# Kernel tuning notes

Measured on AMD Instinct MI355X. Metric: run time of the kernel, lower is better.

## Reference

```python
import jax, jax.numpy as jnp
import numpy as np

WS = 7          # window size (Wh == Ww)
NUM_HEADS = 4

def _relative_position_index(ws):
    coords = np.stack(np.meshgrid(np.arange(ws), np.arange(ws), indexing='ij'))  # (2, ws, ws)
    cf = coords.reshape(2, -1)                                # (2, N)
    rel = cf[:, :, None] - cf[:, None, :]                     # (2, N, N)
    rel = rel.transpose(1, 2, 0)                              # (N, N, 2)
    rel[:, :, 0] += ws - 1
    rel[:, :, 1] += ws - 1
    rel[:, :, 0] *= 2 * ws - 1
    return rel.sum(-1)                                        # (N, N) int

REL_IDX = jnp.asarray(_relative_position_index(WS))


def setup_inputs() -> dict:
    key = jax.random.key(0)
    ks = jax.random.split(key, 7)
    B, C, H, W = 4096, 128, WS, WS
    nW = 64
    N = H * W
    return {
        'x': jax.random.normal(ks[0], (B, C, H, W), jnp.float32),
        'mask': jax.random.normal(ks[1], (nW, 1, N, N), jnp.float32),
        'qkv_w': jax.random.normal(ks[2], (3 * C, C), jnp.float32) * 0.02,
        'qkv_b': jax.random.normal(ks[3], (3 * C,), jnp.float32) * 0.02,
        'proj_w': jax.random.normal(ks[4], (C, C), jnp.float32) * 0.02,
        'proj_b': jax.random.normal(ks[5], (C,), jnp.float32) * 0.02,
        'bias_table': jax.random.normal(ks[6], ((2 * WS - 1) ** 2, NUM_HEADS), jnp.float32) * 0.02,
    }


def reference(x, mask, qkv_w, qkv_b, proj_w, proj_b, bias_table):
    B, C, H, W = x.shape
    N = H * W
    heads = NUM_HEADS
    hd = C // heads
    scale = jnp.asarray(hd, x.dtype) ** -0.5

    # 1x1 conv qkv: (B,C,H,W) -> (B,3C,H,W), then to (B,N,3C)
    qkv = jnp.einsum('bchw,oc->bhwo', x, qkv_w) + qkv_b      # (B,H,W,3C)
    qkv = qkv.reshape(B, N, 3, heads, hd)                     # split channel into q/k/v
    q, k, v = (qkv[:, :, i].transpose(0, 2, 1, 3) for i in range(3))  # each (B,heads,N,hd)

    attn = jnp.einsum('bhnd,bhmd->bhnm', q * scale, k)        # (B,heads,N,N)

    rel_bias = bias_table[REL_IDX.reshape(-1)].reshape(N, N, heads)
    attn = attn + rel_bias.transpose(2, 0, 1)[None]           # (1,heads,N,N) broadcast

    nW = mask.shape[0]
    attn = attn + jnp.tile(mask, (B // nW, 1, 1, 1))          # (B,1,N,N) broadcast over heads

    attn = jax.nn.softmax(attn, axis=-1)
    out = jnp.einsum('bhnm,bhmd->bhnd', attn, v)              # (B,heads,N,hd)
    out = out.transpose(0, 2, 1, 3).reshape(B, N, C)          # (B,N,C)
    out = out.transpose(0, 2, 1).reshape(B, C, H, W)

    # 1x1 proj conv
    out = jnp.einsum('bchw,oc->bohw', out, proj_w) + proj_b[None, :, None, None]
    return out
```

## Files before the change

### kernel.cpp

```cpp
#include <hip/hip_runtime.h>

typedef __attribute__((ext_vector_type(8))) short short8;
typedef __attribute__((ext_vector_type(4))) float f32x4;
typedef __attribute__((ext_vector_type(4))) unsigned short bfu4;

#define MFMA(a, b, c) __builtin_amdgcn_mfma_f32_16x16x32_bf16((a), (b), (c), 0, 0, 0)

__device__ __forceinline__ unsigned short f2bf(float f) {
    union { float f; unsigned u; } v; v.f = f;
    unsigned r = v.u + 0x7fffu + ((v.u >> 16) & 1u);
    return (unsigned short)(r >> 16);
}

__global__ __launch_bounds__(256)
void prep_kernel(const float* __restrict__ qkv_w, const float* __restrict__ proj_w,
                 unsigned short* __restrict__ wf)
{
    int id = blockIdx.x * 256 + threadIdx.x;
    int j  = id & 7;
    int l  = (id >> 3) & 63;
    int ks = (id >> 9) & 3;
    int row16 = l & 15;
    int kk = ks * 32 + ((l >> 4) << 3) + j;
    if (id < 49152) {
        int mt = id >> 11;
        wf[id] = f2bf(qkv_w[(mt * 16 + row16) * 128 + kk]);
    } else {
        int mt = (id - 49152) >> 11;
        wf[id] = f2bf(proj_w[(mt * 16 + row16) * 128 + kk]);
    }
}

#define XS 0
#define QKO 16384
#define VTO 49152
#define PPO 0
#define AOO 32768
#define LDS_BYTES 65536
#define SCALE 0.17677669529663687f

__global__ __launch_bounds__(256, 2)
void win_attn_mfma(const float* __restrict__ x, const float* __restrict__ mask,
                   const float* __restrict__ qkv_b, const float* __restrict__ proj_b,
                   const float* __restrict__ bt, const unsigned short* __restrict__ wf,
                   float* __restrict__ out)
{
    extern __shared__ char smem[];
    const int b = blockIdx.x, tid = threadIdx.x;
    const int w = tid >> 6, l = tid & 63, g = l >> 4, lr = l & 15;

    const float* xb = x + (size_t)b * 6272;
    for (int r = tid; r < 6272; r += 256) {
        int c = (int)(((unsigned)r * 21400u) >> 20);
        int n = r - c * 49;
        int byte = n * 256 + ((c * 2) ^ ((n & 7) << 4));
        *(unsigned short*)(smem + XS + byte) = f2bf(xb[r]);
    }
    for (int i = tid; i < 1920; i += 256) {
        int n = 49 + (i >> 7), c = i & 127;
        int byte = n * 256 + ((c * 2) ^ ((n & 7) << 4));
        *(unsigned short*)(smem + XS + byte) = 0;
    }
    __syncthreads();

    const short8* wfa = (const short8*)wf;

    {
        f32x4 acc[6][4];
        #pragma unroll
        for (int mt = 0; mt < 6; ++mt)
            #pragma unroll
            for (int nt = 0; nt < 4; ++nt) acc[mt][nt] = (f32x4){0.f, 0.f, 0.f, 0.f};

        #pragma unroll
        for (int ks = 0; ks < 4; ++ks) {
            short8 aF[6], bF[4];
            #pragma unroll
            for (int mt = 0; mt < 6; ++mt)
                aF[mt] = wfa[((w * 6 + mt) * 4 + ks) * 64 + l];
            #pragma unroll
            for (int nt = 0; nt < 4; ++nt) {
                int n = nt * 16 + lr;
                int byte = n * 256 + (((ks * 32 + g * 8) * 2) ^ ((n & 7) << 4));
                bF[nt] = *(const short8*)(smem + XS + byte);
            }
            #pragma unroll
            for (int mt = 0; mt < 6; ++mt)
                #pragma unroll
                for (int nt = 0; nt < 4; ++nt)
                    acc[mt][nt] = MFMA(aF[mt], bF[nt], acc[mt][nt]);
        }

        #pragma unroll
        for (int mt = 0; mt < 6; ++mt) {
            int o0 = w * 96 + mt * 16;
            f32x4 bias = *(const f32x4*)(qkv_b + o0 + g * 4);
            #pragma unroll
            for (int nt = 0; nt < 4; ++nt) acc[mt][nt] += bias;

            if (o0 < 128) {
                int hh = o0 >> 5, dl = (o0 & 31) + g * 4;
                #pragma unroll
                for (int nt = 0; nt < 4; ++nt) {
                    int n = nt * 16 + lr;
                    bfu4 u;
                    #pragma unroll
                    for (int r2 = 0; r2 < 4; ++r2) u[r2] = f2bf(acc[mt][nt][r2] * SCALE);
                    int byte = hh * 8192 + n * 128 + ((dl * 2) ^ ((n & 7) << 4));
                    *(bfu4*)(smem + QKO + byte) = u;
                }
            } else if (o0 < 256) {
                int o2 = o0 - 128, hh = o2 >> 5, dl = (o2 & 31) + g * 4;
                #pragma unroll
                for (int nt = 0; nt < 4; ++nt) {
                    int n = nt * 16 + lr;
                    bfu4 u;
                    #pragma unroll
                    for (int r2 = 0; r2 < 4; ++r2) u[r2] = f2bf(acc[mt][nt][r2]);
                    int byte = hh * 8192 + n * 128 + ((64 + dl * 2) ^ ((n & 7) << 4));
                    *(bfu4*)(smem + QKO + byte) = u;
                }
            } else {
                int o2 = o0 - 256, hh = o2 >> 5, dl = (o2 & 31) + g * 4;
                #pragma unroll
                for (int nt = 0; nt < 4; ++nt) {
                    int m = nt * 16 + lr;
                    #pragma unroll
                    for (int r2 = 0; r2 < 4; ++r2) {
                        int d = dl + r2;
                        int byte = hh * 4096 + d * 128 + ((m * 2) ^ ((d & 7) << 4));
                        *(unsigned short*)(smem + VTO + byte) = f2bf(acc[mt][nt][r2]);
                    }
                }
            }
        }
    }
    __syncthreads();

    const int h = w, wi = b & 63;
    f32x4 S[4][4];

    {
        int pm[4], mc[4]; bool mv[4];
        #pragma unroll
        for (int nt = 0; nt < 4; ++nt) {
            int m = nt * 16 + lr;
            int m_c = m > 48 ? 48 : m;
            int ym = (m_c * 147) >> 10, xm = m_c - ym * 7;
            pm[nt] = ym * 13 + xm; mc[nt] = m_c; mv[nt] = (m < 49);
        }
        const float* mrow = mask + (size_t)wi * 2401;
        #pragma unroll
        for (int mt = 0; mt < 4; ++mt) {
            #pragma unroll
            for (int r2 = 0; r2 < 4; ++r2) {
                int n = mt * 16 + g * 4 + r2;
                int n_c = n > 48 ? 48 : n;
                int yn = (n_c * 147) >> 10, xn = n_c - yn * 7;
                int pn = yn * 13 + xn;
                const float* mr2 = mrow + n_c * 49;
                #pragma unroll
                for (int nt = 0; nt < 4; ++nt) {
                    S[mt][nt][r2] = mv[nt]
                        ? (mr2[mc[nt]] + bt[(pn - pm[nt] + 84) * 4 + h])
                        : -1e30f;
                }
            }
        }
    }

    {
        short8 qF[4], kF[4];
        #pragma unroll
        for (int t = 0; t < 4; ++t) {
            int n = t * 16 + lr;
            int rb2 = h * 8192 + n * 128, sw = (n & 7) << 4;
            qF[t] = *(const short8*)(smem + QKO + rb2 + ((g * 16) ^ sw));
            kF[t] = *(const short8*)(smem + QKO + rb2 + ((64 + g * 16) ^ sw));
        }
        #pragma unroll
        for (int mt = 0; mt < 4; ++mt)
            #pragma unroll
            for (int nt = 0; nt < 4; ++nt)
                S[mt][nt] = MFMA(qF[mt], kF[nt], S[mt][nt]);
    }

    #pragma unroll
    for (int mt = 0; mt < 4; ++mt) {
        f32x4 mx = S[mt][0];
        #pragma unroll
        for (int nt = 1; nt < 4; ++nt)
            #pragma unroll
            for (int r2 = 0; r2 < 4; ++r2) mx[r2] = fmaxf(mx[r2], S[mt][nt][r2]);
        #pragma unroll
        for (int r2 = 0; r2 < 4; ++r2) {
            float v2 = mx[r2];
            v2 = fmaxf(v2, __shfl_xor(v2, 1));
            v2 = fmaxf(v2, __shfl_xor(v2, 2));
            v2 = fmaxf(v2, __shfl_xor(v2, 4));
            v2 = fmaxf(v2, __shfl_xor(v2, 8));
            mx[r2] = v2;
        }
        f32x4 sum = (f32x4){0.f, 0.f, 0.f, 0.f};
        #pragma unroll
        for (int nt = 0; nt < 4; ++nt)
            #pragma unroll
            for (int r2 = 0; r2 < 4; ++r2) {
                float e = __expf(S[mt][nt][r2] - mx[r2]);
                S[mt][nt][r2] = e; sum[r2] += e;
            }
        #pragma unroll
        for (int r2 = 0; r2 < 4; ++r2) {
            float s2 = sum[r2];
            s2 += __shfl_xor(s2, 1);
            s2 += __shfl_xor(s2, 2);
            s2 += __shfl_xor(s2, 4);
            s2 += __shfl_xor(s2, 8);
            sum[r2] = 1.0f / s2;
        }
        #pragma unroll
        for (int nt = 0; nt < 4; ++nt)
            #pragma unroll
            for (int r2 = 0; r2 < 4; ++r2) S[mt][nt][r2] *= sum[r2];
    }
    __syncthreads();

    #pragma unroll
    for (int mt = 0; mt < 4; ++mt)
        #pragma unroll
        for (int r2 = 0; r2 < 4; ++r2) {
            int n = mt * 16 + g * 4 + r2;
            int rowb = h * 8192 + n * 128, sw = (n & 7) << 4;
            #pragma unroll
            for (int nt = 0; nt < 4; ++nt) {
                int m = nt * 16 + lr;
                *(unsigned short*)(smem + PPO + rowb + ((m * 2) ^ sw)) = f2bf(S[mt][nt][r2]);
            }
        }

    f32x4 O[4][2];
    #pragma unroll
    for (int mt = 0; mt < 4; ++mt)
        #pragma unroll
        for (int nt2 = 0; nt2 < 2; ++nt2) O[mt][nt2] = (f32x4){0.f, 0.f, 0.f, 0.f};
    #pragma unroll
    for (int ks2 = 0; ks2 < 2; ++ks2) {
        short8 pF[4], vF[2];
        #pragma unroll
        for (int mt = 0; mt < 4; ++mt) {
            int n = mt * 16 + lr;
            pF[mt] = *(const short8*)(smem + PPO + h * 8192 + n * 128 +
                                      ((ks2 * 64 + g * 16) ^ ((n & 7) << 4)));
        }
        #pragma unroll
        for (int nt2 = 0; nt2 < 2; ++nt2) {
            int d = nt2 * 16 + lr;
            vF[nt2] = *(const short8*)(smem + VTO + h * 4096 + d * 128 +
                                       ((ks2 * 64 + g * 16) ^ ((d & 7) << 4)));
        }
        #pragma unroll
        for (int mt = 0; mt < 4; ++mt)
            #pragma unroll
            for (int nt2 = 0; nt2 < 2; ++nt2)
                O[mt][nt2] = MFMA(pF[mt], vF[nt2], O[mt][nt2]);
    }
    #pragma unroll
    for (int mt = 0; mt < 4; ++mt)
        #pragma unroll
        for (int nt2 = 0; nt2 < 2; ++nt2)
            #pragma unroll
            for (int r2 = 0; r2 < 4; ++r2) {
                int n = mt * 16 + g * 4 + r2;
                int c = h * 32 + nt2 * 16 + lr;
                *(unsigned short*)(smem + AOO + n * 256 + ((c * 2) ^ ((n & 7) << 4))) =
                    f2bf(O[mt][nt2][r2]);
            }
    __syncthreads();

    f32x4 Pa[4][2];
    #pragma unroll
    for (int mt = 0; mt < 4; ++mt)
        #pragma unroll
        for (int ct = 0; ct < 2; ++ct) Pa[mt][ct] = (f32x4){0.f, 0.f, 0.f, 0.f};
    #pragma unroll
    for (int ks = 0; ks < 4; ++ks) {
        short8 aF[4], bF[2];
        #pragma unroll
        for (int mt = 0; mt < 4; ++mt) {
            int n = mt * 16 + lr;
            aF[mt] = *(const short8*)(smem + AOO + n * 256 +
                                      (((ks * 32 + g * 8) * 2) ^ ((n & 7) << 4)));
        }
        #pragma unroll
        for (int ct = 0; ct < 2; ++ct)
            bF[ct] = wfa[6144 + ((w * 2 + ct) * 4 + ks) * 64 + l];
        #pragma unroll
        for (int mt = 0; mt < 4; ++mt)
            #pragma unroll
            for (int ct = 0; ct < 2; ++ct)
                Pa[mt][ct] = MFMA(aF[mt], bF[ct], Pa[mt][ct]);
    }
    float* ob = out + (size_t)b * 6272;
    #pragma unroll
    for (int ct = 0; ct < 2; ++ct) {
        int co = (w * 2 + ct) * 16 + lr;
        float pb2 = proj_b[co];
        #pragma unroll
        for (int mt = 0; mt < 4; ++mt) {
            int n0 = mt * 16 + g * 4;
            if (mt < 3) {
                #pragma unroll
                for (int r2 = 0; r2 < 4; ++r2)
                    ob[co * 49 + n0 + r2] = Pa[mt][ct][r2] + pb2;
            } else if (g == 0) {
                ob[co * 49 + 48] = Pa[3][ct][0] + pb2;
            }
        }
    }
}

extern "C" void kernel_launch(void* const* d_in, const int* in_sizes, int n_in,
                              void* d_out, int out_size, void* d_ws, size_t ws_size,
                              hipStream_t stream) {
    const float* x      = (const float*)d_in[0];
    const float* mask   = (const float*)d_in[1];
    const float* qkv_w  = (const float*)d_in[2];
    const float* qkv_b  = (const float*)d_in[3];
    const float* proj_w = (const float*)d_in[4];
    const float* proj_b = (const float*)d_in[5];
    const float* btab   = (const float*)d_in[6];
    float* o = (float*)d_out;
    unsigned short* wf = (unsigned short*)d_ws;

    prep_kernel<<<256, 256, 0, stream>>>(qkv_w, proj_w, wf);

    hipFuncSetAttribute(reinterpret_cast<const void*>(win_attn_mfma),
                        hipFuncAttributeMaxDynamicSharedMemorySize, LDS_BYTES);
    win_attn_mfma<<<4096, 256, LDS_BYTES, stream>>>(x, mask, qkv_b, proj_b, btab, wf, o);
}
```

Measured before the change: 173.6 us.

## Process heads in two passes to shrink LDS and double occupancy

Restructures the window attention kernel to compute QKV and attention for two heads per pass, with each wave handling half the query rows of one head. The LDS footprint drops from 64KB to 40KB and launch bounds rise to 4 blocks per CU, targeting higher occupancy and latency hiding. The x load is also vectorised to float4, and the attention output is kept in registers across passes before the projection. The cost is more barriers per block and a second QKV GEMM pass that reloads x fragments, with a risk of register pressure under the tighter launch bound.

```diff
diff --git a/kernel.cpp b/kernel.cpp
--- a/kernel.cpp
+++ b/kernel.cpp
@@ -5,6 +5,7 @@
 typedef __attribute__((ext_vector_type(4))) unsigned short bfu4;
 
 #define MFMA(a, b, c) __builtin_amdgcn_mfma_f32_16x16x32_bf16((a), (b), (c), 0, 0, 0)
+#define SCALE 0.17677669529663687f
 
 __device__ __forceinline__ unsigned short f2bf(float f) {
     union { float f; unsigned u; } v; v.f = f;
@@ -13,8 +14,8 @@
 }
 
 __global__ __launch_bounds__(256)
-void prep_kernel(const float* __restrict__ qkv_w, const float* __restrict__ proj_w,
-                 unsigned short* __restrict__ wf)
+void prep_w(const float* __restrict__ qkv_w, const float* __restrict__ proj_w,
+            unsigned short* __restrict__ wf)
 {
     int id = blockIdx.x * 256 + threadIdx.x;
     int j  = id & 7;
@@ -31,15 +32,11 @@
     }
 }
 
-#define XS 0
 #define QKO 16384
-#define VTO 49152
-#define PPO 0
-#define AOO 32768
-#define LDS_BYTES 65536
-#define SCALE 0.17677669529663687f
-
-__global__ __launch_bounds__(256, 2)
+#define VTO2 32768
+#define LDS_BYTES 40960
+
+__global__ __launch_bounds__(256, 4)
 void win_attn_mfma(const float* __restrict__ x, const float* __restrict__ mask,
                    const float* __restrict__ qkv_b, const float* __restrict__ proj_b,
                    const float* __restrict__ bt, const unsigned short* __restrict__ wf,
@@ -48,248 +45,269 @@
     extern __shared__ char smem[];
     const int b = blockIdx.x, tid = threadIdx.x;
     const int w = tid >> 6, l = tid & 63, g = l >> 4, lr = l & 15;
-
-    const float* xb = x + (size_t)b * 6272;
-    for (int r = tid; r < 6272; r += 256) {
-        int c = (int)(((unsigned)r * 21400u) >> 20);
-        int n = r - c * 49;
-        int byte = n * 256 + ((c * 2) ^ ((n & 7) << 4));
-        *(unsigned short*)(smem + XS + byte) = f2bf(xb[r]);
-    }
-    for (int i = tid; i < 1920; i += 256) {
-        int n = 49 + (i >> 7), c = i & 127;
-        int byte = n * 256 + ((c * 2) ^ ((n & 7) << 4));
-        *(unsigned short*)(smem + XS + byte) = 0;
+    const int wi = b & 63;
+    const int hh = w >> 1;
+    const int nh = w & 1;
+
+    {
+        const float4* xb4 = (const float4*)(x + (size_t)b * 6272);
+        for (int i = tid; i < 1568; i += 256) {
+            float4 v4 = xb4[i];
+            float vals[4] = {v4.x, v4.y, v4.z, v4.w};
+            int r0 = i * 4;
+            #pragma unroll
+            for (int e = 0; e < 4; ++e) {
+                int r = r0 + e;
+                int c = (int)(((unsigned)r * 21400u) >> 20);
+                int n = r - c * 49;
+                *(unsigned short*)(smem + n * 256 + ((c * 2) ^ ((n & 7) << 4))) =
+                    f2bf(vals[e]);
+            }
+        }
+        for (int i = tid; i < 1920; i += 256) {
+            int n = 49 + (i >> 7), c = i & 127;
+            *(unsigned short*)(smem + n * 256 + ((c * 2) ^ ((n & 7) << 4))) = 0;
+        }
     }
     __syncthreads();
 
     const short8* wfa = (const short8*)wf;
-
-    {
-        f32x4 acc[6][4];
-        #pragma unroll
-        for (int mt = 0; mt < 6; ++mt)
-            #pragma unroll
-            for (int nt = 0; nt < 4; ++nt) acc[mt][nt] = (f32x4){0.f, 0.f, 0.f, 0.f};
-
-        #pragma unroll
-        for (int ks = 0; ks < 4; ++ks) {
-            short8 aF[6], bF[4];
-            #pragma unroll
-            for (int mt = 0; mt < 6; ++mt)
-                aF[mt] = wfa[((w * 6 + mt) * 4 + ks) * 64 + l];
-            #pragma unroll
-            for (int nt = 0; nt < 4; ++nt) {
-                int n = nt * 16 + lr;
-                int byte = n * 256 + (((ks * 32 + g * 8) * 2) ^ ((n & 7) << 4));
-                bF[nt] = *(const short8*)(smem + XS + byte);
-            }
-            #pragma unroll
-            for (int mt = 0; mt < 6; ++mt)
-                #pragma unroll
-                for (int nt = 0; nt < 4; ++nt)
-                    acc[mt][nt] = MFMA(aF[mt], bF[nt], acc[mt][nt]);
-        }
-
-        #pragma unroll
-        for (int mt = 0; mt < 6; ++mt) {
-            int o0 = w * 96 + mt * 16;
-            f32x4 bias = *(const f32x4*)(qkv_b + o0 + g * 4);
-            #pragma unroll
-            for (int nt = 0; nt < 4; ++nt) acc[mt][nt] += bias;
-
-            if (o0 < 128) {
-                int hh = o0 >> 5, dl = (o0 & 31) + g * 4;
+    f32x4 Osav[2][2][2];
+
+    #pragma unroll
+    for (int p2 = 0; p2 < 2; ++p2) {
+        #pragma unroll
+        for (int i = 0; i < 3; ++i) {
+            const int j = w * 3 + i;
+            const int typ = j >> 2;
+            const int jj = j & 3;
+            const int ph = jj >> 1;
+            const int blk = jj & 1;
+            const int T = typ * 8 + p2 * 4 + jj;
+            const int ob = T * 16;
+
+            short8 af[4];
+            #pragma unroll
+            for (int ks = 0; ks < 4; ++ks) af[ks] = wfa[(T * 4 + ks) * 64 + l];
+            f32x4 acc[4];
+            #pragma unroll
+            for (int nt = 0; nt < 4; ++nt) acc[nt] = (f32x4){0.f, 0.f, 0.f, 0.f};
+            #pragma unroll
+            for (int ks = 0; ks < 4; ++ks) {
+                #pragma unroll
+                for (int nt = 0; nt < 4; ++nt) {
+                    int n = nt * 16 + lr;
+                    short8 xf = *(const short8*)(smem + n * 256 +
+                                    ((ks * 64 + g * 16) ^ ((n & 7) << 4)));
+                    acc[nt] = MFMA(af[ks], xf, acc[nt]);
+                }
+            }
+            f32x4 bv = *(const f32x4*)(qkv_b + ob + g * 4);
+            #pragma unroll
+            for (int nt = 0; nt < 4; ++nt) acc[nt] += bv;
+
+            if (typ == 0) {
                 #pragma unroll
                 for (int nt = 0; nt < 4; ++nt) {
                     int n = nt * 16 + lr;
                     bfu4 u;
                     #pragma unroll
-                    for (int r2 = 0; r2 < 4; ++r2) u[r2] = f2bf(acc[mt][nt][r2] * SCALE);
-                    int byte = hh * 8192 + n * 128 + ((dl * 2) ^ ((n & 7) << 4));
-                    *(bfu4*)(smem + QKO + byte) = u;
-                }
-            } else if (o0 < 256) {
-                int o2 = o0 - 128, hh = o2 >> 5, dl = (o2 & 31) + g * 4;
+                    for (int r2 = 0; r2 < 4; ++r2) u[r2] = f2bf(acc[nt][r2] * SCALE);
+                    *(bfu4*)(smem + QKO + ph * 8192 + n * 128 +
+                             ((blk * 32 + g * 8) ^ ((n & 7) << 4))) = u;
+                }
+            } else if (typ == 1) {
                 #pragma unroll
                 for (int nt = 0; nt < 4; ++nt) {
                     int n = nt * 16 + lr;
                     bfu4 u;
                     #pragma unroll
-                    for (int r2 = 0; r2 < 4; ++r2) u[r2] = f2bf(acc[mt][nt][r2]);
-                    int byte = hh * 8192 + n * 128 + ((64 + dl * 2) ^ ((n & 7) << 4));
-                    *(bfu4*)(smem + QKO + byte) = u;
+                    for (int r2 = 0; r2 < 4; ++r2) u[r2] = f2bf(acc[nt][r2]);
+                    *(bfu4*)(smem + QKO + ph * 8192 + n * 128 +
+                             ((64 + blk * 32 + g * 8) ^ ((n & 7) << 4))) = u;
                 }
             } else {
-                int o2 = o0 - 256, hh = o2 >> 5, dl = (o2 & 31) + g * 4;
                 #pragma unroll
                 for (int nt = 0; nt < 4; ++nt) {
                     int m = nt * 16 + lr;
                     #pragma unroll
                     for (int r2 = 0; r2 < 4; ++r2) {
-                        int d = dl + r2;
-                        int byte = hh * 4096 + d * 128 + ((m * 2) ^ ((d & 7) << 4));
-                        *(unsigned short*)(smem + VTO + byte) = f2bf(acc[mt][nt][r2]);
+                        int d = blk * 16 + g * 4 + r2;
+                        *(unsigned short*)(smem + VTO2 + ph * 4096 + d * 128 +
+                                           ((m * 2) ^ ((d & 7) << 4))) = f2bf(acc[nt][r2]);
                     }
                 }
             }
         }
-    }
-    __syncthreads();
-
-    const int h = w, wi = b & 63;
-    f32x4 S[4][4];
-
-    {
-        int pm[4], mc[4]; bool mv[4];
-        #pragma unroll
-        for (int nt = 0; nt < 4; ++nt) {
-            int m = nt * 16 + lr;
-            int m_c = m > 48 ? 48 : m;
-            int ym = (m_c * 147) >> 10, xm = m_c - ym * 7;
-            pm[nt] = ym * 13 + xm; mc[nt] = m_c; mv[nt] = (m < 49);
-        }
-        const float* mrow = mask + (size_t)wi * 2401;
-        #pragma unroll
-        for (int mt = 0; mt < 4; ++mt) {
-            #pragma unroll
-            for (int r2 = 0; r2 < 4; ++r2) {
-                int n = mt * 16 + g * 4 + r2;
-                int n_c = n > 48 ? 48 : n;
-                int yn = (n_c * 147) >> 10, xn = n_c - yn * 7;
-                int pn = yn * 13 + xn;
-                const float* mr2 = mrow + n_c * 49;
-                #pragma unroll
-                for (int nt = 0; nt < 4; ++nt) {
-                    S[mt][nt][r2] = mv[nt]
-                        ? (mr2[mc[nt]] + bt[(pn - pm[nt] + 84) * 4 + h])
-                        : -1e30f;
-                }
-            }
-        }
-    }
-
-    {
-        short8 qF[4], kF[4];
-        #pragma unroll
-        for (int t = 0; t < 4; ++t) {
-            int n = t * 16 + lr;
-            int rb2 = h * 8192 + n * 128, sw = (n & 7) << 4;
-            qF[t] = *(const short8*)(smem + QKO + rb2 + ((g * 16) ^ sw));
-            kF[t] = *(const short8*)(smem + QKO + rb2 + ((64 + g * 16) ^ sw));
-        }
-        #pragma unroll
-        for (int mt = 0; mt < 4; ++mt)
-            #pragma unroll
-            for (int nt = 0; nt < 4; ++nt)
-                S[mt][nt] = MFMA(qF[mt], kF[nt], S[mt][nt]);
-    }
-
-    #pragma unroll
-    for (int mt = 0; mt < 4; ++mt) {
-        f32x4 mx = S[mt][0];
-        #pragma unroll
-        for (int nt = 1; nt < 4; ++nt)
-            #pragma unroll
-            for (int r2 = 0; r2 < 4; ++r2) mx[r2] = fmaxf(mx[r2], S[mt][nt][r2]);
-        #pragma unroll
-        for (int r2 = 0; r2 < 4; ++r2) {
-            float v2 = mx[r2];
-            v2 = fmaxf(v2, __shfl_xor(v2, 1));
-            v2 = fmaxf(v2, __shfl_xor(v2, 2));
-            v2 = fmaxf(v2, __shfl_xor(v2, 4));
-            v2 = fmaxf(v2, __shfl_xor(v2, 8));
-            mx[r2] = v2;
-        }
-        f32x4 sum = (f32x4){0.f, 0.f, 0.f, 0.f};
-        #pragma unroll
-        for (int nt = 0; nt < 4; ++nt)
-            #pragma unroll
-            for (int r2 = 0; r2 < 4; ++r2) {
-                float e = __expf(S[mt][nt][r2] - mx[r2]);
-                S[mt][nt][r2] = e; sum[r2] += e;
-            }
-        #pragma unroll
-        for (int r2 = 0; r2 < 4; ++r2) {
-            float s2 = sum[r2];
-            s2 += __shfl_xor(s2, 1);
-            s2 += __shfl_xor(s2, 2);
-            s2 += __shfl_xor(s2, 4);
-            s2 += __shfl_xor(s2, 8);
-            sum[r2] = 1.0f / s2;
-        }
-        #pragma unroll
-        for (int nt = 0; nt < 4; ++nt)
-            #pragma unroll
-            for (int r2 = 0; r2 < 4; ++r2) S[mt][nt][r2] *= sum[r2];
-    }
-    __syncthreads();
-
-    #pragma unroll
-    for (int mt = 0; mt < 4; ++mt)
-        #pragma unroll
-        for (int r2 = 0; r2 < 4; ++r2) {
-            int n = mt * 16 + g * 4 + r2;
-            int rowb = h * 8192 + n * 128, sw = (n & 7) << 4;
+        __syncthreads();
+
+        const int hgl = p2 * 2 + hh;
+        f32x4 S[2][4];
+        {
+            int pm[4], mc[4]; bool mv[4];
             #pragma unroll
             for (int nt = 0; nt < 4; ++nt) {
                 int m = nt * 16 + lr;
-                *(unsigned short*)(smem + PPO + rowb + ((m * 2) ^ sw)) = f2bf(S[mt][nt][r2]);
-            }
-        }
-
-    f32x4 O[4][2];
+                int m_c = m > 48 ? 48 : m;
+                int ym = (m_c * 147) >> 10, xm = m_c - ym * 7;
+                pm[nt] = ym * 13 + xm; mc[nt] = m_c; mv[nt] = (m < 49);
+            }
+            const float* mrow = mask + (size_t)wi * 2401;
+            #pragma unroll
+            for (int mt = 0; mt < 2; ++mt) {
+                #pragma unroll
+                for (int r2 = 0; r2 < 4; ++r2) {
+                    int n = nh * 32 + mt * 16 + g * 4 + r2;
+                    int n_c = n > 48 ? 48 : n;
+                    int yn = (n_c * 147) >> 10, xn = n_c - yn * 7;
+                    int pn = yn * 13 + xn;
+                    const float* mr2 = mrow + n_c * 49;
+                    #pragma unroll
+                    for (int nt = 0; nt < 4; ++nt) {
+                        S[mt][nt][r2] = mv[nt]
+                            ? (mr2[mc[nt]] + bt[(pn - pm[nt] + 84) * 4 + hgl])
+                            : -1e30f;
+                    }
+                }
+            }
+        }
+        {
+            short8 qF[2], kF[4];
+            #pragma unroll
+            for (int t = 0; t < 2; ++t) {
+                int n = nh * 32 + t * 16 + lr;
+                qF[t] = *(const short8*)(smem + QKO + hh * 8192 + n * 128 +
+                                         ((g * 16) ^ ((n & 7) << 4)));
+            }
+            #pragma unroll
+            for (int t = 0; t < 4; ++t) {
+                int m = t * 16 + lr;
+                kF[t] = *(const short8*)(smem + QKO + hh * 8192 + m * 128 +
+                                         ((64 + g * 16) ^ ((m & 7) << 4)));
+            }
+            #pragma unroll
+            for (int mt = 0; mt < 2; ++mt)
+                #pragma unroll
+                for (int nt = 0; nt < 4; ++nt)
+                    S[mt][nt] = MFMA(qF[mt], kF[nt], S[mt][nt]);
+        }
+        #pragma unroll
+        for (int mt = 0; mt < 2; ++mt) {
+            f32x4 mx = S[mt][0];
+            #pragma unroll
+            for (int nt = 1; nt < 4; ++nt)
+                #pragma unroll
+                for (int r2 = 0; r2 < 4; ++r2) mx[r2] = fmaxf(mx[r2], S[mt][nt][r2]);
+            #pragma unroll
+            for (int r2 = 0; r2 < 4; ++r2) {
+                float v2 = mx[r2];
+                v2 = fmaxf(v2, __shfl_xor(v2, 1));
+                v2 = fmaxf(v2, __shfl_xor(v2, 2));
+                v2 = fmaxf(v2, __shfl_xor(v2, 4));
+                v2 = fmaxf(v2, __shfl_xor(v2, 8));
+                mx[r2] = v2;
+            }
+            f32x4 sum = (f32x4){0.f, 0.f, 0.f, 0.f};
+            #pragma unroll
+            for (int nt = 0; nt < 4; ++nt)
+                #pragma unroll
+                for (int r2 = 0; r2 < 4; ++r2) {
+                    float e = __expf(S[mt][nt][r2] - mx[r2]);
+                    S[mt][nt][r2] = e; sum[r2] += e;
+                }
+            #pragma unroll
+            for (int r2 = 0; r2 < 4; ++r2) {
+                float s2 = sum[r2];
+                s2 += __shfl_xor(s2, 1);
+                s2 += __shfl_xor(s2, 2);
+                s2 += __shfl_xor(s2, 4);
+                s2 += __shfl_xor(s2, 8);
+                sum[r2] = 1.0f / s2;
+            }
+            #pragma unroll
+            for (int nt = 0; nt < 4; ++nt)
+                #pragma unroll
+                for (int r2 = 0; r2 < 4; ++r2) S[mt][nt][r2] *= sum[r2];
+        }
+        __syncthreads();
+
+        #pragma unroll
+        for (int mt = 0; mt < 2; ++mt)
+            #pragma unroll
+            for (int r2 = 0; r2 < 4; ++r2) {
+                int n = nh * 32 + mt * 16 + g * 4 + r2;
+                int rowb = QKO + hh * 8192 + n * 128, sw = (n & 7) << 4;
+                #pragma unroll
+                for (int nt = 0; nt < 4; ++nt) {
+                    int m = nt * 16 + lr;
+                    *(unsigned short*)(smem + rowb + ((m * 2) ^ sw)) =
+                        f2bf(S[mt][nt][r2]);
+                }
+            }
+        __syncthreads();
+
+        f32x4 O[2][2];
+        #pragma unroll
+        for (int mt = 0; mt < 2; ++mt)
+            #pragma unroll
+            for (int dt = 0; dt < 2; ++dt) O[mt][dt] = (f32x4){0.f, 0.f, 0.f, 0.f};
+        #pragma unroll
+        for (int ks2 = 0; ks2 < 2; ++ks2) {
+            short8 pf[2], vf[2];
+            #pragma unroll
+            for (int mt = 0; mt < 2; ++mt) {
+                int n = nh * 32 + mt * 16 + lr;
+                pf[mt] = *(const short8*)(smem + QKO + hh * 8192 + n * 128 +
+                                          ((ks2 * 64 + g * 16) ^ ((n & 7) << 4)));
+            }
+            #pragma unroll
+            for (int dt = 0; dt < 2; ++dt) {
+                int d = dt * 16 + lr;
+                vf[dt] = *(const short8*)(smem + VTO2 + hh * 4096 + d * 128 +
+                                          ((ks2 * 64 + g * 16) ^ ((d & 7) << 4)));
+            }
+            #pragma unroll
+            for (int mt = 0; mt < 2; ++mt)
+                #pragma unroll
+                for (int dt = 0; dt < 2; ++dt)
+                    O[mt][dt] = MFMA(pf[mt], vf[dt], O[mt][dt]);
+        }
+        #pragma unroll
+        for (int mt = 0; mt < 2; ++mt)
+            #pragma unroll
+            for (int dt = 0; dt < 2; ++dt) Osav[p2][mt][dt] = O[mt][dt];
+        __syncthreads();
+    }
+
+    #pragma unroll
+    for (int p2 = 0; p2 < 2; ++p2)
+        #pragma unroll
+        for (int mt = 0; mt < 2; ++mt)
+            #pragma unroll
+            for (int dt = 0; dt < 2; ++dt) {
+                int c = (p2 * 2 + hh) * 32 + dt * 16 + lr;
+                #pragma unroll
+                for (int r2 = 0; r2 < 4; ++r2) {
+                    int n = nh * 32 + mt * 16 + g * 4 + r2;
+                    *(unsigned short*)(smem + n * 256 + ((c * 2) ^ ((n & 7) << 4))) =
+                        f2bf(Osav[p2][mt][dt][r2]);
+                }
+            }
+    __syncthreads();
+
+    f32x4 Pa[4][2];
     #pragma unroll
     for (int mt = 0; mt < 4; ++mt)
         #pragma unroll
-        for (int nt2 = 0; nt2 < 2; ++nt2) O[mt][nt2] = (f32x4){0.f, 0.f, 0.f, 0.f};
-    #pragma unroll
-    for (int ks2 = 0; ks2 < 2; ++ks2) {
-        short8 pF[4], vF[2];
+        for (int ct = 0; ct < 2; ++ct) Pa[mt][ct] = (f32x4){0.f, 0.f, 0.f, 0.f};
+    #pragma unroll
+    for (int ks = 0; ks < 4; ++ks) {
+        short8 aF[4], bF[2];
         #pragma unroll
         for (int mt = 0; mt < 4; ++mt) {
             int n = mt * 16 + lr;
-            pF[mt] = *(const short8*)(smem + PPO + h * 8192 + n * 128 +
-                                      ((ks2 * 64 + g * 16) ^ ((n & 7) << 4)));
-        }
-        #pragma unroll
-        for (int nt2 = 0; nt2 < 2; ++nt2) {
-            int d = nt2 * 16 + lr;
-            vF[nt2] = *(const short8*)(smem + VTO + h * 4096 + d * 128 +
-                                       ((ks2 * 64 + g * 16) ^ ((d & 7) << 4)));
-        }
-        #pragma unroll
-        for (int mt = 0; mt < 4; ++mt)
-            #pragma unroll
-            for (int nt2 = 0; nt2 < 2; ++nt2)
-                O[mt][nt2] = MFMA(pF[mt], vF[nt2], O[mt][nt2]);
-    }
-    #pragma unroll
-    for (int mt = 0; mt < 4; ++mt)
-        #pragma unroll
-        for (int nt2 = 0; nt2 < 2; ++nt2)
-            #pragma unroll
-            for (int r2 = 0; r2 < 4; ++r2) {
-                int n = mt * 16 + g * 4 + r2;
-                int c = h * 32 + nt2 * 16 + lr;
-                *(unsigned short*)(smem + AOO + n * 256 + ((c * 2) ^ ((n & 7) << 4))) =
-                    f2bf(O[mt][nt2][r2]);
-            }
-    __syncthreads();
-
-    f32x4 Pa[4][2];
-    #pragma unroll
-    for (int mt = 0; mt < 4; ++mt)
-        #pragma unroll
-        for (int ct = 0; ct < 2; ++ct) Pa[mt][ct] = (f32x4){0.f, 0.f, 0.f, 0.f};
-    #pragma unroll
-    for (int ks = 0; ks < 4; ++ks) {
-        short8 aF[4], bF[2];
-        #pragma unroll
-        for (int mt = 0; mt < 4; ++mt) {
-            int n = mt * 16 + lr;
-            aF[mt] = *(const short8*)(smem + AOO + n * 256 +
-                                      (((ks * 32 + g * 8) * 2) ^ ((n & 7) << 4)));
+            aF[mt] = *(const short8*)(smem + n * 256 +
+                          ((ks * 64 + g * 16) ^ ((n & 7) << 4)));
         }
         #pragma unroll
         for (int ct = 0; ct < 2; ++ct)
@@ -300,7 +318,7 @@
             for (int ct = 0; ct < 2; ++ct)
                 Pa[mt][ct] = MFMA(aF[mt], bF[ct], Pa[mt][ct]);
     }
-    float* ob = out + (size_t)b * 6272;
+    float* obp = out + (size_t)b * 6272;
     #pragma unroll
     for (int ct = 0; ct < 2; ++ct) {
         int co = (w * 2 + ct) * 16 + lr;
@@ -311,9 +329,9 @@
             if (mt < 3) {
                 #pragma unroll
                 for (int r2 = 0; r2 < 4; ++r2)
-                    ob[co * 49 + n0 + r2] = Pa[mt][ct][r2] + pb2;
+                    obp[co * 49 + n0 + r2] = Pa[mt][ct][r2] + pb2;
             } else if (g == 0) {
-                ob[co * 49 + 48] = Pa[3][ct][0] + pb2;
+                obp[co * 49 + 48] = Pa[3][ct][0] + pb2;
             }
         }
     }
@@ -330,11 +348,12 @@
     const float* proj_b = (const float*)d_in[5];
     const float* btab   = (const float*)d_in[6];
     float* o = (float*)d_out;
+
     unsigned short* wf = (unsigned short*)d_ws;
 
-    prep_kernel<<<256, 256, 0, stream>>>(qkv_w, proj_w, wf);
-
-    hipFuncSetAttribute(reinterpret_cast<const void*>(win_attn_mfma),
+    prep_w<<<256, 256, 0, stream>>>(qkv_w, proj_w, wf);
+
+    (void)hipFuncSetAttribute(reinterpret_cast<const void*>(win_attn_mfma),
                         hipFuncAttributeMaxDynamicSharedMemorySize, LDS_BYTES);
     win_attn_mfma<<<4096, 256, LDS_BYTES, stream>>>(x, mask, qkv_b, proj_b, btab, wf, o);
 }
```

New measurement: 285.0 us. 1.64x slower.
